# Kernel tuning notes

Measured on AMD Instinct MI355X. Metric: run time of the kernel, lower is better.

## Reference

```python
import jax, jax.numpy as jnp
import numpy as np
from jax import lax

B, H, W, C = 16, 56, 56, 256
NH = 8
KD = C // NH  # key/head dim = 32
FF = 1024
EPS = 1e-6
SCALE = KD ** -0.5


def _layernorm(x, g, b):
    m = jnp.mean(x, axis=-1, keepdims=True)
    v = jnp.mean(jnp.square(x - m), axis=-1, keepdims=True)
    return (x - m) * lax.rsqrt(v + EPS) * g + b


def _dwconv(x, w, b):
    # x: (B,H,W,Cd), w: (kh,kw,1,Cd) depthwise (groups = Cd), stride 1, SAME padding
    return lax.conv_general_dilated(
        x, w, window_strides=(1, 1), padding='SAME',
        dimension_numbers=('NHWC', 'HWIO', 'NHWC'),
        feature_group_count=x.shape[-1]) + b


def setup_inputs() -> dict:
    key = jax.random.key(0)
    ks = jax.random.split(key, 20)
    r = lambda i, shape, s=0.02: jax.random.normal(ks[i], shape, jnp.float32) * s
    return {
        'x': jax.random.normal(ks[0], (B, H, W, C), jnp.float32),
        'mask_h': jax.random.normal(ks[1], (NH, H, H), jnp.float32),
        'mask_w': jax.random.normal(ks[2], (NH, W, W), jnp.float32),
        # pos: DWConv2d(C, 3, 1, 1)
        'pos_w': r(3, (3, 3, 1, C)), 'pos_b': jnp.zeros((C,), jnp.float32),
        # retention layer norm
        'ln1_g': jnp.ones((C,), jnp.float32), 'ln1_b': jnp.zeros((C,), jnp.float32),
        # MaSA projections (stored as (in, out) so y = x @ W + b)
        'q_w': r(4, (C, C)), 'q_b': jnp.zeros((C,), jnp.float32),
        'k_w': r(5, (C, C)), 'k_b': jnp.zeros((C,), jnp.float32),
        'v_w': r(6, (C, C)), 'v_b': jnp.zeros((C,), jnp.float32),
        # lepe: DWConv2d(C, 5, 1, 2)
        'lepe_w': r(7, (5, 5, 1, C)), 'lepe_b': jnp.zeros((C,), jnp.float32),
        'out_w': r(8, (C, C)), 'out_b': jnp.zeros((C,), jnp.float32),
        # final layer norm
        'ln2_g': jnp.ones((C,), jnp.float32), 'ln2_b': jnp.zeros((C,), jnp.float32),
        # FFN
        'fc1_w': r(9, (C, FF)), 'fc1_b': jnp.zeros((FF,), jnp.float32),
        'fc2_w': r(10, (FF, C)), 'fc2_b': jnp.zeros((C,), jnp.float32),
    }


def _masa(x, mask_h, mask_w, q_w, q_b, k_w, k_b, v_w, v_b, lepe_w, lepe_b, out_w, out_b):
    b, h, w, _ = x.shape
    q = x @ q_w + q_b
    k = (x @ k_w + k_b) * SCALE
    v = x @ v_w + v_b
    lepe = _dwconv(v, lepe_w, lepe_b)
    qh = q.reshape(b, h, w, NH, KD)
    kh = k.reshape(b, h, w, NH, KD)
    vh = v.reshape(b, h, w, NH, KD)
    # width-axis retention: scores (b, h, NH, w, w), mask_w broadcasts as (NH, w, w)
    attn_w = jax.nn.softmax(jnp.einsum('bhqnd,bhknd->bhnqk', qh, kh) + mask_w, axis=-1)
    vw = jnp.einsum('bhnqk,bhknd->bhnqd', attn_w, vh)  # (b, h, NH, w, KD)
    # height-axis retention: scores (b, w, NH, h, h), mask_h broadcasts as (NH, h, h)
    attn_h = jax.nn.softmax(jnp.einsum('bqwnd,bkwnd->bwnqk', qh, kh) + mask_h, axis=-1)
    out = jnp.einsum('bwnqk,bknwd->bqwnd', attn_h, vw)  # (b, h, w, NH, KD)
    out = out.reshape(b, h, w, NH * KD) + lepe
    return out @ out_w + out_b


def reference(x, mask_h, mask_w, pos_w, pos_b, ln1_g, ln1_b,
              q_w, q_b, k_w, k_b, v_w, v_b, lepe_w, lepe_b, out_w, out_b,
              ln2_g, ln2_b, fc1_w, fc1_b, fc2_w, fc2_b):
    # RetBlock (retention='whole', no layerscale, no dropout / drop_path)
    x = x + _dwconv(x, pos_w, pos_b)
    x = x + _masa(_layernorm(x, ln1_g, ln1_b), mask_h, mask_w,
                  q_w, q_b, k_w, k_b, v_w, v_b, lepe_w, lepe_b, out_w, out_b)
    y = _layernorm(x, ln2_g, ln2_b)
    y = jax.nn.gelu(y @ fc1_w + fc1_b, approximate=False) @ fc2_w + fc2_b
    return x + y
```

## Files before the change

### kernel.cpp

```cpp
#include <hip/hip_runtime.h>
#include <hip/hip_bf16.h>
#include <math.h>
#include <stdint.h>

typedef __bf16 bf16;
typedef __bf16 bf16x8 __attribute__((ext_vector_type(8)));
typedef __bf16 bf16x4 __attribute__((ext_vector_type(4)));
typedef float f32x4 __attribute__((ext_vector_type(4)));

#define NPIX (16*56*56)
#define CH 256
#define SCALE_K 0.17677669529663687f

__global__ void wt_kernel(const float* __restrict__ w, float scale, int K, int N,
                          bf16* __restrict__ out)
{
    int total = K * N;
    for (int idx = blockIdx.x * blockDim.x + threadIdx.x; idx < total;
         idx += gridDim.x * blockDim.x) {
        int n = idx / K, k = idx - n * K;
        out[idx] = (bf16)(w[(size_t)k * N + n] * scale);
    }
}

__global__ void qkv_bias_kernel(const float* __restrict__ qb,
                                const float* __restrict__ kb,
                                const float* __restrict__ vb,
                                float* __restrict__ out)
{
    int i = blockIdx.x * blockDim.x + threadIdx.x;
    if (i < 256) out[i] = qb[i];
    else if (i < 512) out[i] = kb[i - 256] * SCALE_K;
    else if (i < 768) out[i] = vb[i - 512];
}

__global__ __launch_bounds__(256) void posconv_ln_kernel(
    const float* __restrict__ x, const float* __restrict__ w,
    const float* __restrict__ bias, const float* __restrict__ g,
    const float* __restrict__ bta, float* __restrict__ x1,
    bf16* __restrict__ tln)
{
    const int wave = threadIdx.x >> 6, lane = threadIdx.x & 63;
    const long pix = (long)blockIdx.x * 4 + wave;
    const int ww = (int)(pix % 56);
    const int hh = (int)((pix / 56) % 56);
    const int b  = (int)(pix / 3136);
    const int c  = lane * 4;
    float4 acc = ((const float4*)(bias + c))[0];
    float4 xin = ((const float4*)(x + pix * 256 + c))[0];
    acc.x += xin.x; acc.y += xin.y; acc.z += xin.z; acc.w += xin.w;
    #pragma unroll
    for (int dh = 0; dh < 3; ++dh) {
        int h2 = hh + dh - 1;
        if (h2 < 0 || h2 >= 56) continue;
        #pragma unroll
        for (int dw = 0; dw < 3; ++dw) {
            int w2 = ww + dw - 1;
            if (w2 < 0 || w2 >= 56) continue;
            float4 xv = ((const float4*)(x + (((long)(b * 56 + h2)) * 56 + w2) * 256 + c))[0];
            float4 wv = ((const float4*)(w + (dh * 3 + dw) * 256 + c))[0];
            acc.x += xv.x * wv.x; acc.y += xv.y * wv.y;
            acc.z += xv.z * wv.z; acc.w += xv.w * wv.w;
        }
    }
    ((float4*)(x1 + pix * 256 + c))[0] = acc;
    float s  = acc.x + acc.y + acc.z + acc.w;
    float q2 = acc.x * acc.x + acc.y * acc.y + acc.z * acc.z + acc.w * acc.w;
    #pragma unroll
    for (int o = 32; o; o >>= 1) {
        s  += __shfl_xor(s,  o, 64);
        q2 += __shfl_xor(q2, o, 64);
    }
    float mean = s * (1.0f / 256.0f);
    float var  = q2 * (1.0f / 256.0f) - mean * mean;
    float rs   = rsqrtf(var + 1e-6f);
    float4 gv = ((const float4*)g)[lane];
    float4 bv = ((const float4*)bta)[lane];
    bf16* o4 = tln + pix * 256 + c;
    o4[0] = (bf16)((acc.x - mean) * rs * gv.x + bv.x);
    o4[1] = (bf16)((acc.y - mean) * rs * gv.y + bv.y);
    o4[2] = (bf16)((acc.z - mean) * rs * gv.z + bv.z);
    o4[3] = (bf16)((acc.w - mean) * rs * gv.w + bv.w);
}

__global__ __launch_bounds__(256) void lepe_kernel(
    const bf16* __restrict__ qkv, const float* __restrict__ w,
    const float* __restrict__ bias, bf16* __restrict__ out)
{
    long idx = (long)blockIdx.x * 256 + threadIdx.x;
    int c8 = (int)(idx & 31);
    long pix = idx >> 5;
    int ww = (int)(pix % 56);
    int hh = (int)((pix / 56) % 56);
    int b  = (int)(pix / 3136);
    int c  = c8 * 8;
    float acc[8];
    #pragma unroll
    for (int j = 0; j < 8; ++j) acc[j] = bias[c + j];
    #pragma unroll
    for (int dh = 0; dh < 5; ++dh) {
        int h2 = hh + dh - 2;
        if (h2 < 0 || h2 >= 56) continue;
        #pragma unroll
        for (int dw = 0; dw < 5; ++dw) {
            int w2 = ww + dw - 2;
            if (w2 < 0 || w2 >= 56) continue;
            bf16x8 vv = *(const bf16x8*)(qkv + (((long)(b * 56 + h2)) * 56 + w2) * 768 + 512 + c);
            const float4* wp = (const float4*)(w + (dh * 5 + dw) * 256 + c);
            float4 w0 = wp[0], w1 = wp[1];
            acc[0] += (float)vv[0] * w0.x; acc[1] += (float)vv[1] * w0.y;
            acc[2] += (float)vv[2] * w0.z; acc[3] += (float)vv[3] * w0.w;
            acc[4] += (float)vv[4] * w1.x; acc[5] += (float)vv[5] * w1.y;
            acc[6] += (float)vv[6] * w1.z; acc[7] += (float)vv[7] * w1.w;
        }
    }
    bf16* o = out + pix * 256 + c;
    #pragma unroll
    for (int j = 0; j < 8; ++j) o[j] = (bf16)acc[j];
}

template<bool WIDTH>
__global__ __launch_bounds__(256) void attn_mfma_kernel(
    const bf16* __restrict__ qkv, const bf16* __restrict__ vsrc,
    const float* __restrict__ mask, const bf16* __restrict__ lepe,
    bf16* __restrict__ outp)
{
    __shared__ bf16 VtAll[4][32][72];
    __shared__ bf16 PlAll[4][16][72];
    const int tid = threadIdx.x;
    const int wave = tid >> 6, lane = tid & 63;
    const int g = lane >> 4, ql = lane & 15;
    const int n  = blockIdx.x / 224;
    const int s  = (blockIdx.x % 224) * 4 + wave;
    const int b  = s / 56, rc = s % 56;
    bf16 (*Vt)[72] = VtAll[wave];
    bf16 (*Pl)[72] = PlAll[wave];
    const long basePix = WIDTH ? ((long)(b * 56 + rc)) * 56 : (long)b * 3136 + rc;
    const long pixStride = WIDTH ? 1 : 56;
    const bf16* qb = qkv + basePix * 768 + n * 32;
    const long qstride = pixStride * 768;
    const bf16* vbp; long vstride;
    if (WIDTH) { vbp = qb + 512; vstride = qstride; }
    else       { vbp = vsrc + basePix * 256 + n * 32; vstride = pixStride * 256; }

    #pragma unroll
    for (int it = 0; it < 2; ++it) {
        int idx = it * 64 + lane;
        if (idx < 112) {
            int pp = idx >> 2, chunk = idx & 3;
            int pos0 = pp * 2;
            bf16x8 v0 = *(const bf16x8*)(vbp + (long)pos0 * vstride + chunk * 8);
            bf16x8 v1 = *(const bf16x8*)(vbp + (long)(pos0 + 1) * vstride + chunk * 8);
            int colb = pos0 ^ (chunk << 3);
            #pragma unroll
            for (int j = 0; j < 8; ++j) {
                union { bf16 h[2]; unsigned int u; } pk;
                pk.h[0] = v0[j]; pk.h[1] = v1[j];
                *(unsigned int*)&Vt[chunk * 8 + j][colb] = pk.u;
            }
        }
    }
    if (lane < 32) {
        int d = lane;
        int colb = 56 ^ ((d >> 3) << 3);
        *(float4*)&Vt[d][colb] = (float4){0.f, 0.f, 0.f, 0.f};
    }

    bf16x8 qf[4], kf[4];
    #pragma unroll
    for (int t4 = 0; t4 < 4; ++t4) {
        int row = ql + 16 * t4; if (row > 55) row = 55;
        qf[t4] = *(const bf16x8*)(qb + (long)row * qstride + 8 * g);
        kf[t4] = *(const bf16x8*)(qb + (long)row * qstride + 256 + 8 * g);
    }

    f32x4 sA[4][4];
    #pragma unroll
    for (int qt = 0; qt < 4; ++qt)
        #pragma unroll
        for (int kt = 0; kt < 4; ++kt)
            sA[qt][kt] = __builtin_amdgcn_mfma_f32_16x16x32_bf16(
                kf[kt], qf[qt], (f32x4){0.f, 0.f, 0.f, 0.f}, 0, 0, 0);

    const float* mrow = mask + n * 3136;
    #pragma unroll
    for (int qt = 0; qt < 4; ++qt) {
        int qm = ql + 16 * qt; if (qm > 55) qm = 55;
        #pragma unroll
        for (int kt = 0; kt < 4; ++kt) {
            if (kt == 3 && g >= 2) {
                sA[qt][3][0] = -3.0e38f; sA[qt][3][1] = -3.0e38f;
                sA[qt][3][2] = -3.0e38f; sA[qt][3][3] = -3.0e38f;
            } else {
                float4 mv = *(const float4*)(mrow + qm * 56 + kt * 16 + 4 * g);
                sA[qt][kt][0] += mv.x; sA[qt][kt][1] += mv.y;
                sA[qt][kt][2] += mv.z; sA[qt][kt][3] += mv.w;
            }
        }
    }

    #pragma unroll
    for (int qt = 0; qt < 4; ++qt) {
        float m = -3.0e38f;
        #pragma unroll
        for (int kt = 0; kt < 4; ++kt)
            #pragma unroll
            for (int r = 0; r < 4; ++r) m = fmaxf(m, sA[qt][kt][r]);
        m = fmaxf(m, __shfl_xor(m, 16, 64));
        m = fmaxf(m, __shfl_xor(m, 32, 64));
        float p[4][4];
        float sum = 0.f;
        #pragma unroll
        for (int kt = 0; kt < 4; ++kt)
            #pragma unroll
            for (int r = 0; r < 4; ++r) {
                float e = exp2f((sA[qt][kt][r] - m) * 1.4426950408889634f);
                p[kt][r] = e; sum += e;
            }
        sum += __shfl_xor(sum, 16, 64);
        sum += __shfl_xor(sum, 32, 64);
        float rinv = 1.0f / sum;
        #pragma unroll
        for (int kt = 0; kt < 4; ++kt) {
            bf16x4 w;
            #pragma unroll
            for (int r = 0; r < 4; ++r) w[r] = (bf16)(p[kt][r] * rinv);
            *(bf16x4*)&Pl[ql][kt * 16 + 4 * g] = w;
        }
        #pragma unroll
        for (int nt = 0; nt < 2; ++nt) {
            f32x4 o = {0.f, 0.f, 0.f, 0.f};
            #pragma unroll
            for (int ks = 0; ks < 2; ++ks) {
                bf16x8 af = *(const bf16x8*)&Pl[ql][ks * 32 + 8 * g];
                int vrow = ql + 16 * nt;
                int vcol = (ks * 32 + 8 * g) ^ ((vrow >> 3) << 3);
                bf16x8 bv = *(const bf16x8*)&Vt[vrow][vcol];
                o = __builtin_amdgcn_mfma_f32_16x16x32_bf16(af, bv, o, 0, 0, 0);
            }
            if (!(qt == 3 && g >= 2)) {
                #pragma unroll
                for (int r = 0; r < 4; ++r) {
                    int q = 16 * qt + 4 * g + r;
                    long addr = (basePix + (long)q * pixStride) * 256 + n * 32 + nt * 16 + ql;
                    float vv = o[r];
                    if (!WIDTH) vv += (float)lepe[addr];
                    outp[addr] = (bf16)vv;
                }
            }
        }
    }
}

template<bool GELU, bool RESID, bool OUT_BF16>
__global__ __launch_bounds__(256) void gemm_kernel(
    const bf16* __restrict__ A, const bf16* __restrict__ Wt,
    const float* __restrict__ bias, const float* __restrict__ resid,
    void* __restrict__ Cout, int M, int N, int K)
{
    __shared__ bf16 smem[17408];
    bf16* As = smem;
    bf16* Bs = smem + 8192;
    const int t = threadIdx.x;
    const int wave = t >> 6, lane = t & 63;
    const int nTilesN = N >> 7;
    const int q8 = gridDim.x >> 3;
    const int o = ((int)blockIdx.x & 7) * q8 + ((int)blockIdx.x >> 3);
    const int tm = o / nTilesN, tn = o % nTilesN;
    const long m0 = (long)tm * 128, n0 = (long)tn * 128;
    const int waveM = (wave >> 1) * 64, waveN = (wave & 1) * 64;
    f32x4 acc[4][4] = {};

    for (int k0 = 0; k0 < K; k0 += 64) {
        #pragma unroll
        for (int i = 0; i < 4; ++i) {
            int c = i * 256 + wave * 64 + lane;
            int r = c >> 3, cc = (c & 7) * 8;
            const bf16* ga = A  + (m0 + r) * (long)K + k0 + cc;
            const bf16* gb = Wt + (n0 + r) * (long)K + k0 + cc;
            __builtin_amdgcn_global_load_lds(
                (const __attribute__((address_space(1))) void*)ga,
                (__attribute__((address_space(3))) void*)(As + (i * 256 + wave * 64) * 8),
                16, 0, 0);
            __builtin_amdgcn_global_load_lds(
                (const __attribute__((address_space(1))) void*)gb,
                (__attribute__((address_space(3))) void*)(Bs + (i * 256 + wave * 64) * 8),
                16, 0, 0);
        }
        __syncthreads();
        #pragma unroll
        for (int kk = 0; kk < 2; ++kk) {
            bf16x8 af[4], bfr[4];
            const int krow = kk * 32 + (lane >> 4) * 8;
            #pragma unroll
            for (int fm = 0; fm < 4; ++fm)
                af[fm] = *(const bf16x8*)&As[(waveM + fm * 16 + (lane & 15)) * 64 + krow];
            #pragma unroll
            for (int fn = 0; fn < 4; ++fn)
                bfr[fn] = *(const bf16x8*)&Bs[(waveN + fn * 16 + (lane & 15)) * 64 + krow];
            #pragma unroll
            for (int fm = 0; fm < 4; ++fm)
                #pragma unroll
                for (int fn = 0; fn < 4; ++fn)
                    acc[fm][fn] = __builtin_amdgcn_mfma_f32_16x16x32_bf16(
                        af[fm], bfr[fn], acc[fm][fn], 0, 0, 0);
        }
        __syncthreads();
    }

    if constexpr (OUT_BF16) {
        #pragma unroll
        for (int fm = 0; fm < 4; ++fm) {
            #pragma unroll
            for (int r = 0; r < 4; ++r) {
                const int mrow = waveM + fm * 16 + (lane >> 4) * 4 + r;
                #pragma unroll
                for (int fn = 0; fn < 4; ++fn) {
                    const int ncol = waveN + fn * 16 + (lane & 15);
                    float vv = acc[fm][fn][r] + bias[n0 + ncol];
                    if (GELU) {
                        float u = vv * (0.7978845608028654f + 0.0356774081f * vv * vv);
                        float tgh = 1.0f - 2.0f / (__expf(2.0f * u) + 1.0f);
                        vv = 0.5f * vv * (1.0f + tgh);
                    }
                    smem[mrow * 136 + ncol] = (bf16)vv;
                }
            }
        }
        __syncthreads();
        const int rrow = t >> 4, rchunk = t & 15;
        #pragma unroll
        for (int s = 0; s < 8; ++s) {
            int row = s * 16 + rrow;
            bf16x8 val = *(const bf16x8*)&smem[row * 136 + rchunk * 8];
            *(bf16x8*)((bf16*)Cout + (m0 + row) * (long)N + n0 + rchunk * 8) = val;
        }
    } else {
        #pragma unroll
        for (int fm = 0; fm < 4; ++fm) {
            #pragma unroll
            for (int r = 0; r < 4; ++r) {
                const long m = m0 + waveM + fm * 16 + (lane >> 4) * 4 + r;
                #pragma unroll
                for (int fn = 0; fn < 4; ++fn) {
                    const long n = n0 + waveN + fn * 16 + (lane & 15);
                    float vv = acc[fm][fn][r] + bias[n];
                    if (RESID) vv += resid[m * N + n];
                    ((float*)Cout)[m * N + n] = vv;
                }
            }
        }
    }
}

__global__ __launch_bounds__(256) void outln_kernel(
    const bf16* __restrict__ A, const bf16* __restrict__ Wt,
    const float* __restrict__ bias, const float* __restrict__ resid,
    const float* __restrict__ g2, const float* __restrict__ b2,
    float* __restrict__ x2out, bf16* __restrict__ uout)
{
    __shared__ bf16 As[128 * 64];
    __shared__ bf16 Bs[256 * 64];
    const int t = threadIdx.x;
    const int wave = t >> 6, lane = t & 63;
    const int g = lane >> 4, ql = lane & 15;
    const int q8 = gridDim.x >> 3;
    const int o = ((int)blockIdx.x & 7) * q8 + ((int)blockIdx.x >> 3);
    const long m0 = (long)o * 128;
    const int waveM = wave * 32;
    f32x4 acc[2][16] = {};

    for (int k0 = 0; k0 < 256; k0 += 64) {
        #pragma unroll
        for (int i = 0; i < 4; ++i) {
            int c = i * 256 + wave * 64 + lane;
            int r = c >> 3, cc = (c & 7) * 8;
            const bf16* ga = A + (m0 + r) * 256 + k0 + cc;
            __builtin_amdgcn_global_load_lds(
                (const __attribute__((address_space(1))) void*)ga,
                (__attribute__((address_space(3))) void*)(As + (i * 256 + wave * 64) * 8),
                16, 0, 0);
        }
        #pragma unroll
        for (int i = 0; i < 8; ++i) {
            int c = i * 256 + wave * 64 + lane;
            int r = c >> 3, cc = (c & 7) * 8;
            const bf16* gb = Wt + r * 256 + k0 + cc;
            __builtin_amdgcn_global_load_lds(
                (const __attribute__((address_space(1))) void*)gb,
                (__attribute__((address_space(3))) void*)(Bs + (i * 256 + wave * 64) * 8),
                16, 0, 0);
        }
        __syncthreads();
        #pragma unroll
        for (int kk = 0; kk < 2; ++kk) {
            const int krow = kk * 32 + g * 8;
            bf16x8 af[2];
            af[0] = *(const bf16x8*)&As[(waveM + ql) * 64 + krow];
            af[1] = *(const bf16x8*)&As[(waveM + 16 + ql) * 64 + krow];
            #pragma unroll
            for (int fn = 0; fn < 16; ++fn) {
                bf16x8 bv = *(const bf16x8*)&Bs[(fn * 16 + ql) * 64 + krow];
                acc[0][fn] = __builtin_amdgcn_mfma_f32_16x16x32_bf16(af[0], bv, acc[0][fn], 0, 0, 0);
                acc[1][fn] = __builtin_amdgcn_mfma_f32_16x16x32_bf16(af[1], bv, acc[1][fn], 0, 0, 0);
            }
        }
        __syncthreads();
    }

    float rsum[2][4] = {}, rsq[2][4] = {};
    #pragma unroll
    for (int fm = 0; fm < 2; ++fm) {
        #pragma unroll
        for (int fn = 0; fn < 16; ++fn) {
            const int n = fn * 16 + ql;
            const float bn = bias[n];
            #pragma unroll
            for (int r = 0; r < 4; ++r) {
                const long m = m0 + waveM + fm * 16 + g * 4 + r;
                float v = acc[fm][fn][r] + bn + resid[m * 256 + n];
                acc[fm][fn][r] = v;
                rsum[fm][r] += v; rsq[fm][r] += v * v;
            }
        }
    }
    #pragma unroll
    for (int fm = 0; fm < 2; ++fm)
        #pragma unroll
        for (int r = 0; r < 4; ++r) {
            float s = rsum[fm][r], q = rsq[fm][r];
            #pragma unroll
            for (int off = 8; off; off >>= 1) {
                s += __shfl_xor(s, off, 64);
                q += __shfl_xor(q, off, 64);
            }
            float mean = s * (1.0f / 256.0f);
            float var  = q * (1.0f / 256.0f) - mean * mean;
            rsum[fm][r] = mean;
            rsq[fm][r]  = rsqrtf(var + 1e-6f);
        }
    #pragma unroll
    for (int fm = 0; fm < 2; ++fm) {
        #pragma unroll
        for (int fn = 0; fn < 16; ++fn) {
            const int n = fn * 16 + ql;
            const float gn = g2[n], bn2 = b2[n];
            #pragma unroll
            for (int r = 0; r < 4; ++r) {
                const long m = m0 + waveM + fm * 16 + g * 4 + r;
                float v = acc[fm][fn][r];
                x2out[m * 256 + n] = v;
                uout[m * 256 + n] = (bf16)((v - rsum[fm][r]) * rsq[fm][r] * gn + bn2);
            }
        }
    }
}

extern "C" void kernel_launch(void* const* d_in, const int* in_sizes, int n_in,
                              void* d_out, int out_size, void* d_ws, size_t ws_size,
                              hipStream_t stream)
{
    (void)in_sizes; (void)n_in; (void)out_size; (void)ws_size;
    const float* x      = (const float*)d_in[0];
    const float* mask_h = (const float*)d_in[1];
    const float* mask_w = (const float*)d_in[2];
    const float* pos_w  = (const float*)d_in[3];
    const float* pos_b  = (const float*)d_in[4];
    const float* ln1_g  = (const float*)d_in[5];
    const float* ln1_b  = (const float*)d_in[6];
    const float* q_w    = (const float*)d_in[7];
    const float* q_b    = (const float*)d_in[8];
    const float* k_w    = (const float*)d_in[9];
    const float* k_b    = (const float*)d_in[10];
    const float* v_w    = (const float*)d_in[11];
    const float* v_b    = (const float*)d_in[12];
    const float* lepe_w = (const float*)d_in[13];
    const float* lepe_b = (const float*)d_in[14];
    const float* out_w  = (const float*)d_in[15];
    const float* out_b  = (const float*)d_in[16];
    const float* ln2_g  = (const float*)d_in[17];
    const float* ln2_b  = (const float*)d_in[18];
    const float* fc1_w  = (const float*)d_in[19];
    const float* fc1_b  = (const float*)d_in[20];
    const float* fc2_w  = (const float*)d_in[21];
    const float* fc2_b  = (const float*)d_in[22];

    char* ws = (char*)d_ws;
    size_t off = 0;
    auto alloc = [&](size_t bytes) -> void* {
        void* p = ws + off;
        off += (bytes + 255) & ~(size_t)255;
        return p;
    };
    const int M = NPIX;
    float* x1     = (float*)alloc((size_t)M * 256 * 4);
    bf16*  tln    = (bf16*) alloc((size_t)M * 256 * 2);
    bf16*  qkv    = (bf16*) alloc((size_t)M * 768 * 2);
    bf16*  lepeb  = (bf16*) alloc((size_t)M * 256 * 2);
    bf16*  vwb    = (bf16*) alloc((size_t)M * 256 * 2);
    bf16*  obuf   = (bf16*) alloc((size_t)M * 256 * 2);
    bf16*  wt_qkv = (bf16*) alloc((size_t)768 * 256 * 2);
    bf16*  wt_out = (bf16*) alloc((size_t)256 * 256 * 2);
    bf16*  wt_fc1 = (bf16*) alloc((size_t)1024 * 256 * 2);
    bf16*  wt_fc2 = (bf16*) alloc((size_t)256 * 1024 * 2);
    float* qkvb   = (float*)alloc(768 * 4);
    bf16*  h1     = tln;
    float* outf   = (float*)d_out;

    wt_kernel<<<256, 256, 0, stream>>>(q_w, 1.0f, 256, 256, wt_qkv);
    wt_kernel<<<256, 256, 0, stream>>>(k_w, SCALE_K, 256, 256, wt_qkv + 256 * 256);
    wt_kernel<<<256, 256, 0, stream>>>(v_w, 1.0f, 256, 256, wt_qkv + 512 * 256);
    wt_kernel<<<256, 256, 0, stream>>>(out_w, 1.0f, 256, 256, wt_out);
    wt_kernel<<<1024, 256, 0, stream>>>(fc1_w, 1.0f, 256, 1024, wt_fc1);
    wt_kernel<<<1024, 256, 0, stream>>>(fc2_w, 1.0f, 1024, 256, wt_fc2);
    qkv_bias_kernel<<<3, 256, 0, stream>>>(q_b, k_b, v_b, qkvb);

    posconv_ln_kernel<<<12544, 256, 0, stream>>>(x, pos_w, pos_b, ln1_g, ln1_b, x1, tln);
    gemm_kernel<false, false, true><<<392 * 6, 256, 0, stream>>>(
        tln, wt_qkv, qkvb, nullptr, qkv, M, 768, 256);
    lepe_kernel<<<6272, 256, 0, stream>>>(qkv, lepe_w, lepe_b, lepeb);
    attn_mfma_kernel<true><<<1792, 256, 0, stream>>>(qkv, nullptr, mask_w, nullptr, vwb);
    attn_mfma_kernel<false><<<1792, 256, 0, stream>>>(qkv, vwb, mask_h, lepeb, obuf);
    outln_kernel<<<392, 256, 0, stream>>>(
        obuf, wt_out, out_b, x1, ln2_g, ln2_b, outf, lepeb);
    gemm_kernel<true, false, true><<<392 * 8, 256, 0, stream>>>(
        lepeb, wt_fc1, fc1_b, nullptr, h1, M, 1024, 256);
    gemm_kernel<false, true, false><<<392 * 2, 256, 0, stream>>>(
        h1, wt_fc2, fc2_b, outf, outf, M, 256, 1024);
}
```

Before: 449.0 us.

## Simplify GEMM epilogue, use fast exp2 GELU, halve outln tile rows

The GEMM epilogue no longer stages bf16 outputs through shared memory for coalesced 16-byte stores. It now writes scalar bf16 values straight from the accumulators, which shrinks the LDS footprint and removes a barrier. The tanh GELU is rewritten as a sigmoid form using exp2 and hardware reciprocal intrinsics. The out-projection+LN kernel uses 64-row tiles with 784 blocks instead of 128-row tiles, cutting accumulator registers for more parallelism at the cost of reloading the full weight tile per block. The uncoalesced bf16 stores may hurt the QKV and FC1 GEMMs.

```diff
diff --git a/kernel.cpp b/kernel.cpp
--- a/kernel.cpp
+++ b/kernel.cpp
@@ -11,6 +11,12 @@
 #define NPIX (16*56*56)
 #define CH 256
 #define SCALE_K 0.17677669529663687f
+
+__device__ __forceinline__ float gelu_fast(float vv) {
+    float t = vv * (-2.30220781f + -0.10294330f * vv * vv);
+    float e = __builtin_amdgcn_exp2f(t);
+    return vv * __builtin_amdgcn_rcpf(1.0f + e);
+}
 
 __global__ void wt_kernel(const float* __restrict__ w, float scale, int K, int N,
                           bf16* __restrict__ out)
@@ -258,9 +264,8 @@
     const float* __restrict__ bias, const float* __restrict__ resid,
     void* __restrict__ Cout, int M, int N, int K)
 {
-    __shared__ bf16 smem[17408];
-    bf16* As = smem;
-    bf16* Bs = smem + 8192;
+    __shared__ bf16 As[128 * 64];
+    __shared__ bf16 Bs[128 * 64];
     const int t = threadIdx.x;
     const int wave = t >> 6, lane = t & 63;
     const int nTilesN = N >> 7;
@@ -308,46 +313,19 @@
         __syncthreads();
     }
 
-    if constexpr (OUT_BF16) {
-        #pragma unroll
-        for (int fm = 0; fm < 4; ++fm) {
-            #pragma unroll
-            for (int r = 0; r < 4; ++r) {
-                const int mrow = waveM + fm * 16 + (lane >> 4) * 4 + r;
-                #pragma unroll
-                for (int fn = 0; fn < 4; ++fn) {
-                    const int ncol = waveN + fn * 16 + (lane & 15);
-                    float vv = acc[fm][fn][r] + bias[n0 + ncol];
-                    if (GELU) {
-                        float u = vv * (0.7978845608028654f + 0.0356774081f * vv * vv);
-                        float tgh = 1.0f - 2.0f / (__expf(2.0f * u) + 1.0f);
-                        vv = 0.5f * vv * (1.0f + tgh);
-                    }
-                    smem[mrow * 136 + ncol] = (bf16)vv;
-                }
-            }
-        }
-        __syncthreads();
-        const int rrow = t >> 4, rchunk = t & 15;
-        #pragma unroll
-        for (int s = 0; s < 8; ++s) {
-            int row = s * 16 + rrow;
-            bf16x8 val = *(const bf16x8*)&smem[row * 136 + rchunk * 8];
-            *(bf16x8*)((bf16*)Cout + (m0 + row) * (long)N + n0 + rchunk * 8) = val;
-        }
-    } else {
-        #pragma unroll
-        for (int fm = 0; fm < 4; ++fm) {
-            #pragma unroll
-            for (int r = 0; r < 4; ++r) {
-                const long m = m0 + waveM + fm * 16 + (lane >> 4) * 4 + r;
-                #pragma unroll
-                for (int fn = 0; fn < 4; ++fn) {
-                    const long n = n0 + waveN + fn * 16 + (lane & 15);
-                    float vv = acc[fm][fn][r] + bias[n];
-                    if (RESID) vv += resid[m * N + n];
-                    ((float*)Cout)[m * N + n] = vv;
-                }
+    #pragma unroll
+    for (int fm = 0; fm < 4; ++fm) {
+        #pragma unroll
+        for (int r = 0; r < 4; ++r) {
+            const long m = m0 + waveM + fm * 16 + (lane >> 4) * 4 + r;
+            #pragma unroll
+            for (int fn = 0; fn < 4; ++fn) {
+                const long n = n0 + waveN + fn * 16 + (lane & 15);
+                float vv = acc[fm][fn][r] + bias[n];
+                if (GELU)  vv = gelu_fast(vv);
+                if (RESID) vv += resid[m * N + n];
+                if (OUT_BF16) ((bf16*)Cout)[m * N + n] = (bf16)vv;
+                else          ((float*)Cout)[m * N + n] = vv;
             }
         }
     }
@@ -359,20 +337,20 @@
     const float* __restrict__ g2, const float* __restrict__ b2,
     float* __restrict__ x2out, bf16* __restrict__ uout)
 {
-    __shared__ bf16 As[128 * 64];
+    __shared__ bf16 As[64 * 64];
     __shared__ bf16 Bs[256 * 64];
     const int t = threadIdx.x;
     const int wave = t >> 6, lane = t & 63;
     const int g = lane >> 4, ql = lane & 15;
     const int q8 = gridDim.x >> 3;
     const int o = ((int)blockIdx.x & 7) * q8 + ((int)blockIdx.x >> 3);
-    const long m0 = (long)o * 128;
-    const int waveM = wave * 32;
-    f32x4 acc[2][16] = {};
+    const long m0 = (long)o * 64;
+    const int waveM = wave * 16;
+    f32x4 acc[16] = {};
 
     for (int k0 = 0; k0 < 256; k0 += 64) {
         #pragma unroll
-        for (int i = 0; i < 4; ++i) {
+        for (int i = 0; i < 2; ++i) {
             int c = i * 256 + wave * 64 + lane;
             int r = c >> 3, cc = (c & 7) * 8;
             const bf16* ga = A + (m0 + r) * 256 + k0 + cc;
@@ -395,63 +373,52 @@
         #pragma unroll
         for (int kk = 0; kk < 2; ++kk) {
             const int krow = kk * 32 + g * 8;
-            bf16x8 af[2];
-            af[0] = *(const bf16x8*)&As[(waveM + ql) * 64 + krow];
-            af[1] = *(const bf16x8*)&As[(waveM + 16 + ql) * 64 + krow];
+            bf16x8 af = *(const bf16x8*)&As[(waveM + ql) * 64 + krow];
             #pragma unroll
             for (int fn = 0; fn < 16; ++fn) {
                 bf16x8 bv = *(const bf16x8*)&Bs[(fn * 16 + ql) * 64 + krow];
-                acc[0][fn] = __builtin_amdgcn_mfma_f32_16x16x32_bf16(af[0], bv, acc[0][fn], 0, 0, 0);
-                acc[1][fn] = __builtin_amdgcn_mfma_f32_16x16x32_bf16(af[1], bv, acc[1][fn], 0, 0, 0);
+                acc[fn] = __builtin_amdgcn_mfma_f32_16x16x32_bf16(af, bv, acc[fn], 0, 0, 0);
             }
         }
         __syncthreads();
     }
 
-    float rsum[2][4] = {}, rsq[2][4] = {};
-    #pragma unroll
-    for (int fm = 0; fm < 2; ++fm) {
-        #pragma unroll
-        for (int fn = 0; fn < 16; ++fn) {
-            const int n = fn * 16 + ql;
-            const float bn = bias[n];
-            #pragma unroll
-            for (int r = 0; r < 4; ++r) {
-                const long m = m0 + waveM + fm * 16 + g * 4 + r;
-                float v = acc[fm][fn][r] + bn + resid[m * 256 + n];
-                acc[fm][fn][r] = v;
-                rsum[fm][r] += v; rsq[fm][r] += v * v;
-            }
-        }
-    }
-    #pragma unroll
-    for (int fm = 0; fm < 2; ++fm)
+    float rsum[4] = {}, rsq[4] = {};
+    #pragma unroll
+    for (int fn = 0; fn < 16; ++fn) {
+        const int n = fn * 16 + ql;
+        const float bn = bias[n];
         #pragma unroll
         for (int r = 0; r < 4; ++r) {
-            float s = rsum[fm][r], q = rsq[fm][r];
-            #pragma unroll
-            for (int off = 8; off; off >>= 1) {
-                s += __shfl_xor(s, off, 64);
-                q += __shfl_xor(q, off, 64);
-            }
-            float mean = s * (1.0f / 256.0f);
-            float var  = q * (1.0f / 256.0f) - mean * mean;
-            rsum[fm][r] = mean;
-            rsq[fm][r]  = rsqrtf(var + 1e-6f);
-        }
-    #pragma unroll
-    for (int fm = 0; fm < 2; ++fm) {
-        #pragma unroll
-        for (int fn = 0; fn < 16; ++fn) {
-            const int n = fn * 16 + ql;
-            const float gn = g2[n], bn2 = b2[n];
-            #pragma unroll
-            for (int r = 0; r < 4; ++r) {
-                const long m = m0 + waveM + fm * 16 + g * 4 + r;
-                float v = acc[fm][fn][r];
-                x2out[m * 256 + n] = v;
-                uout[m * 256 + n] = (bf16)((v - rsum[fm][r]) * rsq[fm][r] * gn + bn2);
-            }
+            const long m = m0 + waveM + g * 4 + r;
+            float v = acc[fn][r] + bn + resid[m * 256 + n];
+            acc[fn][r] = v;
+            rsum[r] += v; rsq[r] += v * v;
+        }
+    }
+    #pragma unroll
+    for (int r = 0; r < 4; ++r) {
+        float s = rsum[r], q = rsq[r];
+        #pragma unroll
+        for (int off = 8; off; off >>= 1) {
+            s += __shfl_xor(s, off, 64);
+            q += __shfl_xor(q, off, 64);
+        }
+        float mean = s * (1.0f / 256.0f);
+        float var  = q * (1.0f / 256.0f) - mean * mean;
+        rsum[r] = mean;
+        rsq[r]  = rsqrtf(var + 1e-6f);
+    }
+    #pragma unroll
+    for (int fn = 0; fn < 16; ++fn) {
+        const int n = fn * 16 + ql;
+        const float gn = g2[n], bn2 = b2[n];
+        #pragma unroll
+        for (int r = 0; r < 4; ++r) {
+            const long m = m0 + waveM + g * 4 + r;
+            float v = acc[fn][r];
+            x2out[m * 256 + n] = v;
+            uout[m * 256 + n] = (bf16)((v - rsum[r]) * rsq[r] * gn + bn2);
         }
     }
 }
@@ -521,7 +488,7 @@
     lepe_kernel<<<6272, 256, 0, stream>>>(qkv, lepe_w, lepe_b, lepeb);
     attn_mfma_kernel<true><<<1792, 256, 0, stream>>>(qkv, nullptr, mask_w, nullptr, vwb);
     attn_mfma_kernel<false><<<1792, 256, 0, stream>>>(qkv, vwb, mask_h, lepeb, obuf);
-    outln_kernel<<<392, 256, 0, stream>>>(
+    outln_kernel<<<784, 256, 0, stream>>>(
         obuf, wt_out, out_b, x1, ln2_g, ln2_b, outf, lepeb);
     gemm_kernel<true, false, true><<<392 * 8, 256, 0, stream>>>(
         lepeb, wt_fc1, fc1_b, nullptr, h1, M, 1024, 256);
```

Measured after the change: 428.5 us. 4.6% less time.
